# Optimization experiments

Measured on AMD Instinct MI355X. Metric: run time of the kernel, lower is better.

The kernel has to match this reference:

```python
import jax, jax.numpy as jnp
import numpy as np

TEXT_DIM = 4096
FEATURE_DIM = 4096


def _xavier_uniform(key, shape):
    fan_in, fan_out = shape[1], shape[0]
    limit = float(np.sqrt(6.0 / (fan_in + fan_out)))
    return jax.random.uniform(key, shape, jnp.float32, -limit, limit)


def setup_inputs() -> dict:
    key = jax.random.key(0)
    k1, k2, k3, k4 = jax.random.split(key, 4)
    text = jax.random.normal(k1, (8, 2048, TEXT_DIM), jnp.float32)
    features = jax.random.normal(k2, (8, 576, FEATURE_DIM), jnp.float32)
    # nn.Linear weights: [out, in]; biases initialized to 0
    Wq = _xavier_uniform(k3, (FEATURE_DIM, TEXT_DIM))
    bq = jnp.zeros((FEATURE_DIM,), jnp.float32)
    Wk = _xavier_uniform(k4, (FEATURE_DIM, FEATURE_DIM))
    bk = jnp.zeros((FEATURE_DIM,), jnp.float32)
    return {"text": text, "features": features, "Wq": Wq, "bq": bq, "Wk": Wk, "bk": bk}


def reference(text, features, Wq, bq, Wk, bk):
    # Q: [b, t, d], K: [b, p, d]
    Q = jnp.einsum('btx,dx->btd', text, Wq) + bq
    K = jnp.einsum('bpx,dx->bpd', features, Wk) + bk
    scale = 1.0 / jnp.sqrt(jnp.asarray(K.shape[-1], K.dtype))
    scores = jnp.einsum('btd,bpd->btp', Q, K) * scale  # [b, t, p]
    attn = jax.nn.softmax(scores, axis=-1)
    attended = jnp.einsum('btp,bpd->btd', attn, features)  # [b, t, d]
    return attended
```

## Files before the change

kernel.cpp:

```cpp
#include <hip/hip_runtime.h>
#include <hip/hip_bf16.h>
#include <stdint.h>

#define DEVI __device__ __forceinline__

typedef __attribute__((ext_vector_type(8))) __bf16 bf16x8;
typedef __attribute__((ext_vector_type(4))) float f32x4;

DEVI unsigned short f2b(float f) {
  union { float f; unsigned int u; } x; x.f = f;
  unsigned int u = x.u;
  return (unsigned short)((u + 0x7fffu + ((u >> 16) & 1u)) >> 16);
}

DEVI float b2f(unsigned short b) {
  union { unsigned int u; float f; } x; x.u = (unsigned int)b << 16;
  return x.f;
}

__global__ void cvt_kernel(const float* __restrict__ in,
                           unsigned short* __restrict__ out, long n4) {
  long i = (long)blockIdx.x * blockDim.x + threadIdx.x;
  long stride = (long)gridDim.x * blockDim.x;
  for (; i < n4; i += stride) {
    float4 v = reinterpret_cast<const float4*>(in)[i];
    ushort4 o;
    o.x = f2b(v.x); o.y = f2b(v.y); o.z = f2b(v.z); o.w = f2b(v.w);
    reinterpret_cast<ushort4*>(out)[i] = o;
  }
}

__global__ void transpose_cvt_kernel(const float* __restrict__ in,
                                     unsigned short* __restrict__ out,
                                     int P, int D) {
  __shared__ unsigned short tile[32][33];
  int b = blockIdx.z;
  int d0 = blockIdx.x * 32, p0 = blockIdx.y * 32;
  const float* src = in + (long)b * P * D;
  unsigned short* dst = out + (long)b * D * P;
  int tx = threadIdx.x & 31, ty = threadIdx.x >> 5;
  for (int i = 0; i < 32; i += 8)
    tile[ty + i][tx] = f2b(src[(long)(p0 + ty + i) * D + d0 + tx]);
  __syncthreads();
  for (int i = 0; i < 32; i += 8)
    dst[(long)(d0 + ty + i) * P + p0 + tx] = tile[tx][ty + i];
}

__global__ void feat_cvt_tr_kernel(const float* __restrict__ in,
                                   unsigned short* __restrict__ outN,
                                   unsigned short* __restrict__ outT,
                                   int P, int D) {
  __shared__ unsigned short tile[32][33];
  int b = blockIdx.z;
  int d0 = blockIdx.x * 32, p0 = blockIdx.y * 32;
  const float* src = in + (long)b * P * D;
  unsigned short* dstN = outN + (long)b * P * D;
  unsigned short* dstT = outT + (long)b * D * P;
  int tx = threadIdx.x & 31, ty = threadIdx.x >> 5;
  for (int i = 0; i < 32; i += 8) {
    unsigned short v = f2b(src[(long)(p0 + ty + i) * D + d0 + tx]);
    tile[ty + i][tx] = v;
    dstN[(long)(p0 + ty + i) * D + d0 + tx] = v;
  }
  __syncthreads();
  for (int i = 0; i < 32; i += 8)
    dstT[(long)(d0 + ty + i) * P + p0 + tx] = tile[tx][ty + i];
}

__global__ void rowdot_bf16_kernel(const unsigned short* __restrict__ A,
                                   const float* __restrict__ v,
                                   float* __restrict__ out, int D) {
  long row = (long)blockIdx.x * 4 + (threadIdx.x >> 6);
  int lane = threadIdx.x & 63;
  const ushort4* ar = (const ushort4*)(A + row * D);
  const float4* vv = (const float4*)v;
  float s = 0.f;
  for (int j = lane; j < D / 4; j += 64) {
    ushort4 a = ar[j];
    float4 g = vv[j];
    s += b2f(a.x) * g.x + b2f(a.y) * g.y + b2f(a.z) * g.z + b2f(a.w) * g.w;
  }
#pragma unroll
  for (int o = 32; o > 0; o >>= 1) s += __shfl_xor(s, o, 64);
  if (lane == 0) out[row] = s;
}

DEVI void gll16(const void* g, void* l) {
  __builtin_amdgcn_global_load_lds(
      (const __attribute__((address_space(1))) unsigned int*)g,
      (__attribute__((address_space(3))) unsigned int*)l, 16, 0, 0);
}

template<int OUT_BF16, int HAS_BIAS, int BATCH_X,
         int WM, int WN, int ACCM, int ACCN, int WAVES_EU>
__global__ __launch_bounds__(256, WAVES_EU) void gemm_nt_kernel(
    const unsigned short* __restrict__ A,
    const unsigned short* __restrict__ B,
    void* __restrict__ Cv,
    const float* __restrict__ bias,
    float scale, int M, int N, int K,
    long sA, long sB, long sC, long sBias) {
  constexpr int NW = WM * WN;
  constexpr int SA = WM * ACCM;
  constexpr int SB = WN * ACCN;
  constexpr int CA2 = SA * 2 / NW;
  constexpr int CB2 = SB * 2 / NW;
  static_assert(CA2 * NW == SA * 2 && CB2 * NW == SB * 2, "issue divisibility");

  __shared__ unsigned short As[SA * 1024];
  __shared__ unsigned short Bs[SB * 1024];

  const int tid = threadIdx.x;
  const int lane = tid & 63;
  const int wid = tid >> 6;
  const int wm = wid / WN;
  const int wn = wid % WN;

  int bx = blockIdx.x;
  int b;
  if (BATCH_X) { b = bx & 7; bx >>= 3; } else { b = blockIdx.z; }
  const int n0 = bx * (SB * 16);
  const int m0 = blockIdx.y * (SA * 16);

  const unsigned short* Ab = A + (long)b * sA;
  const unsigned short* Bb = B + (long)b * sB;
  const float* biasb = HAS_BIAS ? bias + (long)b * sBias : nullptr;

  const int r8 = lane >> 3;
  const int csw = ((lane & 7) ^ r8) * 8;

  auto stage = [&](int k0) {
#pragma unroll
    for (int t = 0; t < CA2; ++t) {
      const int a = wid * CA2 + t, j = a >> 1, i = a & 1;
      gll16(Ab + (long)(m0 + j * 16 + i * 8 + r8) * K + k0 + csw,
            (void*)(As + j * 1024 + i * 512));
    }
#pragma unroll
    for (int t = 0; t < CB2; ++t) {
      const int a = wid * CB2 + t, j = a >> 1, i = a & 1;
      gll16(Bb + (long)(n0 + j * 16 + i * 8 + r8) * K + k0 + csw,
            (void*)(Bs + j * 1024 + i * 512));
    }
  };

  f32x4 acc[ACCM][ACCN];
#pragma unroll
  for (int m = 0; m < ACCM; ++m)
#pragma unroll
    for (int n = 0; n < ACCN; ++n) acc[m][n] = (f32x4){0.f, 0.f, 0.f, 0.f};

  const int lrow = lane & 15;
  const int x7 = lane & 7;
  const int g = lane >> 4;
  const int so0 = ((g) ^ x7) * 8;
  const int so1 = ((4 + g) ^ x7) * 8;
  const int wmA = wm * ACCM * 16;
  const int wnB = wn * ACCN * 16;

  for (int k0 = 0; k0 < K; k0 += 64) {
    stage(k0);
    __syncthreads();

#pragma unroll
    for (int s = 0; s < 2; ++s) {
      const int so = s ? so1 : so0;
      bf16x8 af[ACCM], bfr[ACCN];
#pragma unroll
      for (int m = 0; m < ACCM; ++m)
        af[m] = *reinterpret_cast<const bf16x8*>(
            &As[(wmA + m * 16 + lrow) * 64 + so]);
#pragma unroll
      for (int n = 0; n < ACCN; ++n)
        bfr[n] = *reinterpret_cast<const bf16x8*>(
            &Bs[(wnB + n * 16 + lrow) * 64 + so]);
#pragma unroll
      for (int m = 0; m < ACCM; ++m)
#pragma unroll
        for (int n = 0; n < ACCN; ++n)
          acc[m][n] = __builtin_amdgcn_mfma_f32_16x16x32_bf16(af[m], bfr[n], acc[m][n], 0, 0, 0);
    }

    __syncthreads();
  }

  const int crow = (lane >> 4) * 4;
  const int ccol = lane & 15;
#pragma unroll
  for (int m = 0; m < ACCM; ++m) {
#pragma unroll
    for (int n = 0; n < ACCN; ++n) {
      const int gc = n0 + wn * ACCN * 16 + n * 16 + ccol;
      float bv = HAS_BIAS ? biasb[gc] : 0.f;
#pragma unroll
      for (int r = 0; r < 4; ++r) {
        const int gr = m0 + wm * ACCM * 16 + m * 16 + crow + r;
        float v = (acc[m][n][r] + bv) * scale;
        long off = (long)b * sC + (long)gr * N + gc;
        if (OUT_BF16)
          ((unsigned short*)Cv)[off] = f2b(v);
        else
          ((float*)Cv)[off] = v;
      }
    }
  }
}

__global__ void softmax_kernel(const float* __restrict__ s,
                               unsigned short* __restrict__ attn) {
  const int P = 576;
  long row = (long)blockIdx.x * 4 + (threadIdx.x >> 6);
  int lane = threadIdx.x & 63;
  const float* sr = s + row * P;
  unsigned short* ar = attn + row * P;
  float v[9];
  float mx = -3.0e38f;
#pragma unroll
  for (int j = 0; j < 9; ++j) {
    v[j] = sr[j * 64 + lane];
    mx = fmaxf(mx, v[j]);
  }
#pragma unroll
  for (int o = 32; o > 0; o >>= 1) mx = fmaxf(mx, __shfl_xor(mx, o, 64));
  float sum = 0.f;
#pragma unroll
  for (int j = 0; j < 9; ++j) {
    v[j] = __expf(v[j] - mx);
    sum += v[j];
  }
#pragma unroll
  for (int o = 32; o > 0; o >>= 1) sum += __shfl_xor(sum, o, 64);
  float inv = 1.0f / sum;
#pragma unroll
  for (int j = 0; j < 9; ++j) ar[j * 64 + lane] = f2b(v[j] * inv);
}

extern "C" void kernel_launch(void* const* d_in, const int* in_sizes, int n_in,
                              void* d_out, int out_size, void* d_ws, size_t ws_size,
                              hipStream_t stream) {
  const float* text = (const float*)d_in[0];
  const float* feat = (const float*)d_in[1];
  const float* Wq = (const float*)d_in[2];
  const float* bq = (const float*)d_in[3];
  const float* Wk = (const float*)d_in[4];
  const float* bk = (const float*)d_in[5];
  (void)bk;
  (void)Wk;

  const int B = 8, T = 2048, P = 576, D = 4096;
  const long nText = (long)B * T * D;
  const long nFeat = (long)B * P * D;

  char* ws = (char*)d_ws;
  unsigned short* text_b = (unsigned short*)(ws);
  unsigned short* feat_b = (unsigned short*)(ws + 134217728);
  unsigned short* fT_b   = (unsigned short*)(ws + 171966464);
  unsigned short* WqT_b  = (unsigned short*)(ws + 209715200);
  unsigned short* WkT_b  = (unsigned short*)(ws + 243269632);
  unsigned short* attn_b = (unsigned short*)(ws + 276824064);
  float* u               = (float*)(ws + 295698432);
  float* c               = (float*)(ws + 295714816);
  float* scores          = (float*)(ws + 209715200);
  unsigned short* W2T_b  = (unsigned short*)d_out;
  unsigned short* KW_b   = (unsigned short*)((char*)d_out + 67108864);

  dim3 blk(256);
  cvt_kernel<<<4096, blk, 0, stream>>>(text, text_b, nText / 4);
  feat_cvt_tr_kernel<<<dim3(D / 32, P / 32, B), blk, 0, stream>>>(feat, feat_b, fT_b, P, D);
  transpose_cvt_kernel<<<dim3(D / 32, D / 32, 1), blk, 0, stream>>>(Wq, WqT_b, D, D);
  transpose_cvt_kernel<<<dim3(D / 32, D / 32, 1), blk, 0, stream>>>(Wk, WkT_b, D, D);
  rowdot_bf16_kernel<<<D / 4, blk, 0, stream>>>(WkT_b, bq, u, D);
  rowdot_bf16_kernel<<<(B * P) / 4, blk, 0, stream>>>(feat_b, u, c, D);

  gemm_nt_kernel<1, 0, 0, 2, 2, 4, 4, 4><<<dim3(32, 32, 1), blk, 0, stream>>>(
      WqT_b, WkT_b, W2T_b, nullptr, 1.0f, D, D, D, 0, 0, 0, 0);
  gemm_nt_kernel<1, 0, 0, 2, 2, 4, 4, 4><<<dim3(32, 36, 1), blk, 0, stream>>>(
      feat_b, W2T_b, KW_b, nullptr, 1.0f, B * P, D, D, 0, 0, 0, 0);
  gemm_nt_kernel<0, 1, 1, 2, 2, 8, 2, 4><<<dim3(72, 8), blk, 0, stream>>>(
      text_b, KW_b, scores, c, 1.0f / 64.0f, T, P, D,
      (long)T * D, (long)P * D, (long)T * P, P);
  softmax_kernel<<<(B * T) / 4, blk, 0, stream>>>(scores, attn_b);
  gemm_nt_kernel<0, 0, 1, 2, 2, 4, 4, 4><<<dim3(256, 16), blk, 0, stream>>>(
      attn_b, fT_b, (float*)d_out, nullptr, 1.0f, T, D, P,
      (long)T * P, (long)D * P, (long)T * D, 0);
}
```

Baseline: 719.8 us.

## Fuse text fp32-to-bf16 conversion into scores GEMM A-operand load

Removes the standalone text conversion pass by having the scores GEMM read fp32 text directly, convert it to bf16 in registers and write it to shared memory, replacing the async global-to-LDS path for A. It also merges the two weight transpose-conversion launches into one kernel using blockIdx.z. This avoids writing and re-reading a 128MB bf16 copy of text. In exchange the GEMM reads twice as many bytes for A and loses the async direct-to-LDS loads, so A staging now goes through registers.

Result: slower. 912.8 us (+26.8%).

```diff
diff --git a/kernel.cpp b/kernel.cpp
--- a/kernel.cpp
+++ b/kernel.cpp
@@ -16,34 +16,6 @@
 DEVI float b2f(unsigned short b) {
   union { unsigned int u; float f; } x; x.u = (unsigned int)b << 16;
   return x.f;
-}
-
-__global__ void cvt_kernel(const float* __restrict__ in,
-                           unsigned short* __restrict__ out, long n4) {
-  long i = (long)blockIdx.x * blockDim.x + threadIdx.x;
-  long stride = (long)gridDim.x * blockDim.x;
-  for (; i < n4; i += stride) {
-    float4 v = reinterpret_cast<const float4*>(in)[i];
-    ushort4 o;
-    o.x = f2b(v.x); o.y = f2b(v.y); o.z = f2b(v.z); o.w = f2b(v.w);
-    reinterpret_cast<ushort4*>(out)[i] = o;
-  }
-}
-
-__global__ void transpose_cvt_kernel(const float* __restrict__ in,
-                                     unsigned short* __restrict__ out,
-                                     int P, int D) {
-  __shared__ unsigned short tile[32][33];
-  int b = blockIdx.z;
-  int d0 = blockIdx.x * 32, p0 = blockIdx.y * 32;
-  const float* src = in + (long)b * P * D;
-  unsigned short* dst = out + (long)b * D * P;
-  int tx = threadIdx.x & 31, ty = threadIdx.x >> 5;
-  for (int i = 0; i < 32; i += 8)
-    tile[ty + i][tx] = f2b(src[(long)(p0 + ty + i) * D + d0 + tx]);
-  __syncthreads();
-  for (int i = 0; i < 32; i += 8)
-    dst[(long)(d0 + ty + i) * P + p0 + tx] = tile[tx][ty + i];
 }
 
 __global__ void feat_cvt_tr_kernel(const float* __restrict__ in,
@@ -67,6 +39,22 @@
     dstT[(long)(d0 + ty + i) * P + p0 + tx] = tile[tx][ty + i];
 }
 
+__global__ void wtr2_kernel(const float* __restrict__ Wq,
+                            const float* __restrict__ Wk,
+                            unsigned short* __restrict__ WqT,
+                            unsigned short* __restrict__ WkT, int D) {
+  __shared__ unsigned short tile[32][33];
+  const float* src = blockIdx.z ? Wk : Wq;
+  unsigned short* dst = blockIdx.z ? WkT : WqT;
+  int d0 = blockIdx.x * 32, p0 = blockIdx.y * 32;
+  int tx = threadIdx.x & 31, ty = threadIdx.x >> 5;
+  for (int i = 0; i < 32; i += 8)
+    tile[ty + i][tx] = f2b(src[(long)(p0 + ty + i) * D + d0 + tx]);
+  __syncthreads();
+  for (int i = 0; i < 32; i += 8)
+    dst[(long)(d0 + ty + i) * D + p0 + tx] = tile[tx][ty + i];
+}
+
 __global__ void rowdot_bf16_kernel(const unsigned short* __restrict__ A,
                                    const float* __restrict__ v,
                                    float* __restrict__ out, int D) {
@@ -92,9 +80,9 @@
 }
 
 template<int OUT_BF16, int HAS_BIAS, int BATCH_X,
-         int WM, int WN, int ACCM, int ACCN, int WAVES_EU>
+         int WM, int WN, int ACCM, int ACCN, int WAVES_EU, int A_F32>
 __global__ __launch_bounds__(256, WAVES_EU) void gemm_nt_kernel(
-    const unsigned short* __restrict__ A,
+    const void* __restrict__ Av,
     const unsigned short* __restrict__ B,
     void* __restrict__ Cv,
     const float* __restrict__ bias,
@@ -122,7 +110,8 @@
   const int n0 = bx * (SB * 16);
   const int m0 = blockIdx.y * (SA * 16);
 
-  const unsigned short* Ab = A + (long)b * sA;
+  const unsigned short* Ab = A_F32 ? nullptr : (const unsigned short*)Av + (long)b * sA;
+  const float* Afb = A_F32 ? (const float*)Av + (long)b * sA : nullptr;
   const unsigned short* Bb = B + (long)b * sB;
   const float* biasb = HAS_BIAS ? bias + (long)b * sBias : nullptr;
 
@@ -133,8 +122,19 @@
 #pragma unroll
     for (int t = 0; t < CA2; ++t) {
       const int a = wid * CA2 + t, j = a >> 1, i = a & 1;
-      gll16(Ab + (long)(m0 + j * 16 + i * 8 + r8) * K + k0 + csw,
-            (void*)(As + j * 1024 + i * 512));
+      if constexpr (A_F32) {
+        const float* src = Afb + (long)(m0 + j * 16 + i * 8 + r8) * K + k0 + csw;
+        float4 v0 = *reinterpret_cast<const float4*>(src);
+        float4 v1 = *reinterpret_cast<const float4*>(src + 4);
+        ushort4 o0 = { f2b(v0.x), f2b(v0.y), f2b(v0.z), f2b(v0.w) };
+        ushort4 o1 = { f2b(v1.x), f2b(v1.y), f2b(v1.z), f2b(v1.w) };
+        unsigned short* dst = As + j * 1024 + i * 512 + lane * 8;
+        *reinterpret_cast<ushort4*>(dst) = o0;
+        *reinterpret_cast<ushort4*>(dst + 4) = o1;
+      } else {
+        gll16(Ab + (long)(m0 + j * 16 + i * 8 + r8) * K + k0 + csw,
+              (void*)(As + j * 1024 + i * 512));
+      }
     }
 #pragma unroll
     for (int t = 0; t < CB2; ++t) {
@@ -245,14 +245,10 @@
   const float* Wk = (const float*)d_in[4];
   const float* bk = (const float*)d_in[5];
   (void)bk;
-  (void)Wk;
 
   const int B = 8, T = 2048, P = 576, D = 4096;
-  const long nText = (long)B * T * D;
-  const long nFeat = (long)B * P * D;
 
   char* ws = (char*)d_ws;
-  unsigned short* text_b = (unsigned short*)(ws);
   unsigned short* feat_b = (unsigned short*)(ws + 134217728);
   unsigned short* fT_b   = (unsigned short*)(ws + 171966464);
   unsigned short* WqT_b  = (unsigned short*)(ws + 209715200);
@@ -265,22 +261,20 @@
   unsigned short* KW_b   = (unsigned short*)((char*)d_out + 67108864);
 
   dim3 blk(256);
-  cvt_kernel<<<4096, blk, 0, stream>>>(text, text_b, nText / 4);
   feat_cvt_tr_kernel<<<dim3(D / 32, P / 32, B), blk, 0, stream>>>(feat, feat_b, fT_b, P, D);
-  transpose_cvt_kernel<<<dim3(D / 32, D / 32, 1), blk, 0, stream>>>(Wq, WqT_b, D, D);
-  transpose_cvt_kernel<<<dim3(D / 32, D / 32, 1), blk, 0, stream>>>(Wk, WkT_b, D, D);
+  wtr2_kernel<<<dim3(D / 32, D / 32, 2), blk, 0, stream>>>(Wq, Wk, WqT_b, WkT_b, D);
   rowdot_bf16_kernel<<<D / 4, blk, 0, stream>>>(WkT_b, bq, u, D);
   rowdot_bf16_kernel<<<(B * P) / 4, blk, 0, stream>>>(feat_b, u, c, D);
 
-  gemm_nt_kernel<1, 0, 0, 2, 2, 4, 4, 4><<<dim3(32, 32, 1), blk, 0, stream>>>(
+  gemm_nt_kernel<1, 0, 0, 2, 2, 4, 4, 4, 0><<<dim3(32, 32, 1), blk, 0, stream>>>(
       WqT_b, WkT_b, W2T_b, nullptr, 1.0f, D, D, D, 0, 0, 0, 0);
-  gemm_nt_kernel<1, 0, 0, 2, 2, 4, 4, 4><<<dim3(32, 36, 1), blk, 0, stream>>>(
+  gemm_nt_kernel<1, 0, 0, 2, 2, 4, 4, 4, 0><<<dim3(32, 36, 1), blk, 0, stream>>>(
       feat_b, W2T_b, KW_b, nullptr, 1.0f, B * P, D, D, 0, 0, 0, 0);
-  gemm_nt_kernel<0, 1, 1, 2, 2, 8, 2, 4><<<dim3(72, 8), blk, 0, stream>>>(
-      text_b, KW_b, scores, c, 1.0f / 64.0f, T, P, D,
+  gemm_nt_kernel<0, 1, 1, 2, 2, 8, 2, 4, 1><<<dim3(72, 8), blk, 0, stream>>>(
+      text, KW_b, scores, c, 1.0f / 64.0f, T, P, D,
       (long)T * D, (long)P * D, (long)T * P, P);
   softmax_kernel<<<(B * T) / 4, blk, 0, stream>>>(scores, attn_b);
-  gemm_nt_kernel<0, 0, 1, 2, 2, 4, 4, 4><<<dim3(256, 16), blk, 0, stream>>>(
+  gemm_nt_kernel<0, 0, 1, 2, 2, 4, 4, 4, 0><<<dim3(256, 16), blk, 0, stream>>>(
       attn_b, fT_b, (float*)d_out, nullptr, 1.0f, T, D, P,
       (long)T * P, (long)D * P, (long)T * D, 0);
 }
```
